# Kernel optimization log

Hardware: AMD Instinct MI355X
Metric: run time of the kernel (lower is better)

The kernel has to match this reference:

```python
import jax, jax.numpy as jnp
import numpy as np

B, T, C = 4, 2048, 1024
N_HEAD = 16
HEAD = C // N_HEAD

def setup_inputs() -> dict:
    key = jax.random.key(0)
    k1, k2, k3 = jax.random.split(key, 3)
    x = jax.random.normal(k1, (B, T, C), dtype=jnp.float32)
    w_attn = jax.random.normal(k2, (C, 3 * C), dtype=jnp.float32) * (1.0 / np.sqrt(C))
    w_proj = jax.random.normal(k3, (C, C), dtype=jnp.float32) * (1.0 / np.sqrt(C))
    return {"x": x, "w_attn": w_attn, "w_proj": w_proj}

def reference(x, w_attn, w_proj):
    b, t, c = x.shape
    qkv = x @ w_attn  # [B,T,3C]
    q, k, v = jnp.split(qkv, 3, axis=-1)
    # [B,T,C] -> [B,H,T,D]
    def heads(z):
        return z.reshape(b, t, N_HEAD, HEAD).transpose(0, 2, 1, 3)
    q, k, v = heads(q), heads(k), heads(v)
    scale = 1.0 / np.sqrt(HEAD)
    att = jnp.einsum('bhqd,bhkd->bhqk', q, k) * scale  # [B,H,T,T]
    causal = jnp.tril(jnp.ones((t, t), dtype=bool))
    att = jnp.where(causal[None, None], att, -jnp.inf)
    att = jax.nn.softmax(att, axis=-1)
    y = jnp.einsum('bhqk,bhkd->bhqd', att, v)  # [B,H,T,D]
    y = y.transpose(0, 2, 1, 3).reshape(b, t, c)
    return y @ w_proj
```

## Files before the change

### kernel.cpp

```cpp
#include <hip/hip_runtime.h>
#include <hip/hip_bf16.h>


typedef __attribute__((ext_vector_type(8))) short bf16x8;
typedef __attribute__((ext_vector_type(4))) float f32x4;
typedef __attribute__((ext_vector_type(16))) float f32x16;

#define T_DIM 2048
#define NHEAD 16
#define HDIM  64

__device__ __forceinline__ unsigned short f2bf(float f) {
    union { float f; unsigned int u; } v; v.f = f;
    unsigned int r = v.u + 0x7fffu + ((v.u >> 16) & 1u);
    return (unsigned short)(r >> 16);
}

__device__ __forceinline__ unsigned cvtpk_bf16(float lo, float hi) {
    unsigned r;
    asm("v_cvt_pk_bf16_f32 %0, %1, %2" : "=v"(r) : "v"(lo), "v"(hi));
    return r;
}
__device__ __forceinline__ void pl32swap(unsigned &x, unsigned &y) {
    asm("v_permlane32_swap_b32 %0, %1" : "+v"(x), "+v"(y));
}
__device__ __forceinline__ bf16x8 mk8(unsigned w0, unsigned w1, unsigned w2, unsigned w3) {
    union { unsigned u[4]; bf16x8 v; } p;
    p.u[0] = w0; p.u[1] = w1; p.u[2] = w2; p.u[3] = w3;
    return p.v;
}

__device__ __forceinline__ void gload_lds16(const void* g, void* l) {
    __builtin_amdgcn_global_load_lds(
        (const __attribute__((address_space(1))) void*)g,
        (__attribute__((address_space(3))) void*)l,
        16, 0, 0);
}

__global__ void cvt_bf16_k(const float* __restrict__ src, unsigned short* __restrict__ dst, int n) {
    int i = (blockIdx.x * blockDim.x + threadIdx.x) * 4;
    if (i < n) {
        float4 v = *(const float4*)(src + i);
        ushort4 o; o.x = f2bf(v.x); o.y = f2bf(v.y); o.z = f2bf(v.z); o.w = f2bf(v.w);
        *(ushort4*)(dst + i) = o;
    }
}

__global__ void transpose_wb_k(const float* __restrict__ src, unsigned short* __restrict__ dst,
                               int R, int Cc) {
    __shared__ float tile[32][33];
    int c0 = blockIdx.x * 32, r0 = blockIdx.y * 32;
    int tx = threadIdx.x & 31, ty = threadIdx.x >> 5;
    #pragma unroll
    for (int i = 0; i < 32; i += 8)
        tile[ty + i][tx] = src[(size_t)(r0 + ty + i) * Cc + c0 + tx];
    __syncthreads();
    #pragma unroll
    for (int i = 0; i < 32; i += 8)
        dst[(size_t)(c0 + ty + i) * R + r0 + tx] = f2bf(tile[tx][ty + i]);
}

template<int EPI>
__global__ __launch_bounds__(512, 2) void gemm_bt_k(
    const unsigned short* __restrict__ A, const unsigned short* __restrict__ Bt,
    void* __restrict__ out0, void* __restrict__ out1, void* __restrict__ out2,
    int M, int N, int K)
{
    extern __shared__ __align__(16) unsigned short smem[];
    unsigned short* sA = smem;
    unsigned short* sB = smem + 49152;

    const int tid = threadIdx.x, lane = tid & 63, wave = tid >> 6;
    const int wm = wave >> 1, wn = wave & 1;
    const int lrow = lane & 15, hi = lane >> 4;

    const int nwg = gridDim.x * gridDim.y;
    const int lin = blockIdx.y * gridDim.x + blockIdx.x;
    const int lin2 = (lin & 7) * (nwg >> 3) + (lin >> 3);
    const int bxg = lin2 % gridDim.x, byg = lin2 / gridDim.x;
    const int row0 = byg * 256, col0 = bxg * 128;

    const int arow = tid >> 3;
    const int gk = ((tid & 7) ^ (arow & 7)) * 8;
    const unsigned short* gA0 = A + (size_t)(row0 + arow) * K + gk;
    const unsigned short* gA1 = A + (size_t)(row0 + arow + 64) * K + gk;
    const unsigned short* gA2 = A + (size_t)(row0 + arow + 128) * K + gk;
    const unsigned short* gA3 = A + (size_t)(row0 + arow + 192) * K + gk;
    const unsigned short* gB0 = Bt + (size_t)(col0 + arow) * K + gk;
    const unsigned short* gB1 = Bt + (size_t)(col0 + arow + 64) * K + gk;

    const int NT = K >> 6;

#define STAGE(ts, sl) { const size_t ko_ = (size_t)(ts) * 64; \
        unsigned short* dA_ = sA + (sl) * 16384; \
        unsigned short* dB_ = sB + (sl) * 8192; \
        gload_lds16(gA0 + ko_, dA_ + tid * 8); \
        gload_lds16(gA1 + ko_, dA_ + (tid + 512) * 8); \
        gload_lds16(gA2 + ko_, dA_ + (tid + 1024) * 8); \
        gload_lds16(gA3 + ko_, dA_ + (tid + 1536) * 8); \
        gload_lds16(gB0 + ko_, dB_ + tid * 8); \
        gload_lds16(gB1 + ko_, dB_ + (tid + 512) * 8); }

    f32x4 acc[4][4] = {};

    STAGE(0, 0);
    STAGE(1, 1);
    asm volatile("s_waitcnt vmcnt(6)" ::: "memory");
    __builtin_amdgcn_s_barrier();
    __builtin_amdgcn_sched_barrier(0);

    int slot = 0;
    for (int t = 0; t < NT; ++t) {
        if (t + 2 < NT) {
            const int s2 = (slot + 2 >= 3) ? slot - 1 : slot + 2;
            STAGE(t + 2, s2);
        }
        const unsigned short* As = sA + slot * 16384;
        const unsigned short* Bs = sB + slot * 8192;
        bf16x8 af[2][4], bf_[2][4];
        #pragma unroll
        for (int ks = 0; ks < 2; ++ks) {
            const int kc = (ks * 4 + hi) ^ (lrow & 7);
            #pragma unroll
            for (int mi = 0; mi < 4; ++mi)
                af[ks][mi] = *(const bf16x8*)&As[((wm * 64 + mi * 16 + lrow) * 8 + kc) * 8];
            #pragma unroll
            for (int ni = 0; ni < 4; ++ni)
                bf_[ks][ni] = *(const bf16x8*)&Bs[((wn * 64 + ni * 16 + lrow) * 8 + kc) * 8];
        }
        __builtin_amdgcn_s_setprio(1);
        #pragma unroll
        for (int ks = 0; ks < 2; ++ks)
            #pragma unroll
            for (int mi = 0; mi < 4; ++mi)
                #pragma unroll
                for (int ni = 0; ni < 4; ++ni)
                    acc[mi][ni] = __builtin_amdgcn_mfma_f32_16x16x32_bf16(af[ks][mi], bf_[ks][ni], acc[mi][ni], 0, 0, 0);
        __builtin_amdgcn_s_setprio(0);
        if (t + 2 < NT) { asm volatile("s_waitcnt vmcnt(6)" ::: "memory"); }
        else           { asm volatile("s_waitcnt vmcnt(0)" ::: "memory"); }
        __builtin_amdgcn_s_barrier();
        __builtin_amdgcn_sched_barrier(0);
        slot = (slot + 1 >= 3) ? 0 : slot + 1;
    }
#undef STAGE

    if (EPI == 1) {
        #pragma unroll
        for (int mi = 0; mi < 4; ++mi)
            #pragma unroll
            for (int ni = 0; ni < 4; ++ni) {
                int gm0 = row0 + wm * 64 + mi * 16 + hi * 4;
                int gn  = col0 + wn * 64 + ni * 16 + lrow;
                #pragma unroll
                for (int r = 0; r < 4; ++r)
                    ((float*)out0)[(size_t)(gm0 + r) * N + gn] = acc[mi][ni][r];
            }
    } else if (col0 < 1024) {
        const int bb = row0 >> 11;
        #pragma unroll
        for (int mi = 0; mi < 4; ++mi)
            #pragma unroll
            for (int ni = 0; ni < 4; ++ni) {
                int gm0 = row0 + wm * 64 + mi * 16 + hi * 4;
                int gn  = col0 + wn * 64 + ni * 16 + lrow;
                int h = (gn >> 6) & 15, d = gn & 63;
                #pragma unroll
                for (int r = 0; r < 4; ++r) {
                    int t = (gm0 + r) & 2047;
                    ((unsigned short*)out0)[((size_t)(bb * NHEAD + h) * T_DIM + t) * HDIM + d] =
                        f2bf(acc[mi][ni][r] * 0.18033688011112042f);
                }
            }
    } else {
        const bool isK = (col0 < 2048);
        unsigned short* st = smem;
        __syncthreads();
        #pragma unroll
        for (int mi = 0; mi < 4; ++mi) {
            #pragma unroll
            for (int ni = 0; ni < 4; ++ni) {
                const int gnl = wn * 64 + ni * 16 + lrow;
                const int hl = gnl >> 6, d = gnl & 63;
                #pragma unroll
                for (int r = 0; r < 4; ++r) {
                    const int tl = wm * 64 + mi * 16 + hi * 4 + r;
                    int idx;
                    if (isK) idx = (hl * 4 + (tl >> 6)) * 4096 + ((d >> 3) * 64 + (tl & 63)) * 8 + (d & 7);
                    else     idx = (hl * 4 + (tl >> 6)) * 4096 + (((tl >> 3) & 7) * 64 + d) * 8 + (tl & 7);
                    st[idx] = f2bf(acc[mi][ni][r]);
                }
            }
        }
        __syncthreads();
        unsigned short* outb = (unsigned short*)(isK ? out1 : out2);
        const int bb = row0 >> 11;
        const int h0 = (col0 & 1023) >> 6;
        const int tc0 = (row0 & 2047) >> 6;
        #pragma unroll
        for (int seg = 0; seg < 8; ++seg) {
            const int hl = seg >> 2, tc = seg & 3;
            const size_t gbase = ((size_t)(bb * NHEAD + h0 + hl) * 32 + tc0 + tc) * 4096;
            *(uint4*)(outb + gbase + tid * 8) = *(const uint4*)(st + seg * 4096 + tid * 8);
        }
    }
}

__global__ __launch_bounds__(512) void attn_k(
    const unsigned short* __restrict__ qb, const unsigned short* __restrict__ kcm,
    const unsigned short* __restrict__ vcm, unsigned short* __restrict__ yb)
{
    __shared__ __align__(16) unsigned short Ks[2][4096];
    __shared__ __align__(16) unsigned short Vs[2][4096];

    const int tid = threadIdx.x, lane = tid & 63, wave = tid >> 6;
    const int bh = blockIdx.y;
    const int q32 = lane & 31, hi32 = lane >> 5;
    const unsigned short* Kg = kcm + (size_t)bh * 32 * 4096;
    const unsigned short* Vg = vcm + (size_t)bh * 32 * 4096;

    #pragma unroll
    for (int pass = 0; pass < 2; ++pass) {
        const int bxx = (pass == 0) ? (int)blockIdx.x : (7 - (int)blockIdx.x);
        const int ntiles = 4 * bxx + 4;
        const int q0w = bxx * 256 + wave * 32;
        const int qg = q0w + q32;

        const unsigned short* qrow = qb + ((size_t)bh * T_DIM + q0w + q32) * HDIM;
        bf16x8 qf[4];
        #pragma unroll
        for (int kc = 0; kc < 4; ++kc)
            qf[kc] = *(const bf16x8*)(qrow + kc * 16 + hi32 * 8);

        f32x16 o0 = {}, o1 = {};
        float lsum = 0.f;

        gload_lds16(Kg + tid * 8, &Ks[0][tid * 8]);
        gload_lds16(Vg + tid * 8, &Vs[0][tid * 8]);
        __syncthreads();

        int cur = 0;
        for (int jt = 0; jt < ntiles; ++jt) {
            if (jt + 1 < ntiles) {
                gload_lds16(Kg + (size_t)(jt + 1) * 4096 + tid * 8, &Ks[cur ^ 1][tid * 8]);
                gload_lds16(Vg + (size_t)(jt + 1) * 4096 + tid * 8, &Vs[cur ^ 1][tid * 8]);
            }
            if (jt * 64 <= q0w + 31) {
                f32x16 s0 = {}, s1 = {};
                #pragma unroll
                for (int kc = 0; kc < 4; ++kc) {
                    bf16x8 a0 = *(const bf16x8*)&Ks[cur][((kc * 2 + hi32) * 64 + q32) * 8];
                    bf16x8 a1 = *(const bf16x8*)&Ks[cur][((kc * 2 + hi32) * 64 + 32 + q32) * 8];
                    s0 = __builtin_amdgcn_mfma_f32_32x32x16_bf16(a0, qf[kc], s0, 0, 0, 0);
                    s1 = __builtin_amdgcn_mfma_f32_32x32x16_bf16(a1, qf[kc], s1, 0, 0, 0);
                }
                if (jt * 64 + 63 > q0w) {
                    #pragma unroll
                    for (int r = 0; r < 16; ++r) {
                        int kv0 = jt * 64 + (r & 3) + 8 * (r >> 2) + 4 * hi32;
                        if (kv0 > qg)      s0[r] = -1e30f;
                        if (kv0 + 32 > qg) s1[r] = -1e30f;
                    }
                }
                bf16x8 pa[4];
                #pragma unroll
                for (int blk = 0; blk < 2; ++blk) {
                    float p_[16]; unsigned w_[8];
                    #pragma unroll
                    for (int i = 0; i < 16; ++i) {
                        float sv = blk ? s1[i] : s0[i];
                        p_[i] = __builtin_amdgcn_exp2f(sv - 16.0f);
                        lsum += p_[i];
                    }
                    #pragma unroll
                    for (int i = 0; i < 8; ++i) w_[i] = cvtpk_bf16(p_[2 * i], p_[2 * i + 1]);
                    pl32swap(w_[0], w_[2]); pl32swap(w_[1], w_[3]);
                    pl32swap(w_[4], w_[6]); pl32swap(w_[5], w_[7]);
                    pa[blk * 2]     = mk8(w_[0], w_[1], w_[2], w_[3]);
                    pa[blk * 2 + 1] = mk8(w_[4], w_[5], w_[6], w_[7]);
                }
                #pragma unroll
                for (int kvc = 0; kvc < 4; ++kvc) {
                    bf16x8 b0 = *(const bf16x8*)&Vs[cur][((kvc * 2 + hi32) * 64 + q32) * 8];
                    bf16x8 b1 = *(const bf16x8*)&Vs[cur][((kvc * 2 + hi32) * 64 + 32 + q32) * 8];
                    o0 = __builtin_amdgcn_mfma_f32_32x32x16_bf16(pa[kvc], b0, o0, 0, 0, 0);
                    o1 = __builtin_amdgcn_mfma_f32_32x32x16_bf16(pa[kvc], b1, o1, 0, 0, 0);
                }
            }
            __syncthreads();
            cur ^= 1;
        }

        {
            unsigned la = __float_as_uint(lsum), lb = __float_as_uint(lsum);
            pl32swap(la, lb);
            lsum = __uint_as_float(la) + __uint_as_float(lb);
        }
        const int bb2 = bh >> 4, h = bh & 15;
        #pragma unroll
        for (int r = 0; r < 16; ++r) {
            const int cr = (r & 3) + 8 * (r >> 2) + 4 * hi32;
            float inv = 1.0f / __shfl(lsum, cr);
            int t = q0w + cr;
            size_t off = ((size_t)(bb2 * T_DIM + t)) * 1024 + h * HDIM + q32;
            yb[off]      = f2bf(o0[r] * inv);
            yb[off + 32] = f2bf(o1[r] * inv);
        }
    }
}

extern "C" void kernel_launch(void* const* d_in, const int* in_sizes, int n_in,
                              void* d_out, int out_size, void* d_ws, size_t ws_size,
                              hipStream_t stream) {
    const float* x      = (const float*)d_in[0];
    const float* w_attn = (const float*)d_in[1];
    const float* w_proj = (const float*)d_in[2];
    float* out = (float*)d_out;

    unsigned short* xb  = (unsigned short*)d_ws;
    unsigned short* wat = xb  + (size_t)8192 * 1024;
    unsigned short* wpt = wat + (size_t)3072 * 1024;
    unsigned short* qb  = wpt + (size_t)1024 * 1024;
    unsigned short* kcm = qb  + (size_t)64 * 2048 * 64;
    unsigned short* vcm = kcm + (size_t)64 * 2048 * 64;
    unsigned short* yb  = vcm + (size_t)64 * 2048 * 64;

    (void)hipFuncSetAttribute((const void*)gemm_bt_k<0>,
                              hipFuncAttributeMaxDynamicSharedMemorySize, 147456);
    (void)hipFuncSetAttribute((const void*)gemm_bt_k<1>,
                              hipFuncAttributeMaxDynamicSharedMemorySize, 147456);

    cvt_bf16_k<<<8192, 256, 0, stream>>>(x, xb, 8192 * 1024);
    transpose_wb_k<<<dim3(96, 32), 256, 0, stream>>>(w_attn, wat, 1024, 3072);
    transpose_wb_k<<<dim3(32, 32), 256, 0, stream>>>(w_proj, wpt, 1024, 1024);

    gemm_bt_k<0><<<dim3(24, 32), 512, 147456, stream>>>(xb, wat, qb, kcm, vcm, 8192, 3072, 1024);
    attn_k<<<dim3(4, 64), 512, 0, stream>>>(qb, kcm, vcm, yb);
    gemm_bt_k<1><<<dim3(8, 32), 512, 147456, stream>>>(yb, wpt, out, nullptr, nullptr, 8192, 1024, 1024);
}
```

Before: 168.9 us.

## Split GEMM K-step into two half-phases interleaving LDS reads, global prefetch and MFMA

```diff
diff --git a/kernel.cpp b/kernel.cpp
--- a/kernel.cpp
+++ b/kernel.cpp
@@ -91,51 +91,74 @@
 
     const int NT = K >> 6;
 
-#define STAGE(ts, sl) { const size_t ko_ = (size_t)(ts) * 64; \
+#define STAGE_P0(ts, sl) { const size_t ko_ = (size_t)(ts) * 64; \
+        unsigned short* dA_ = sA + (sl) * 16384; \
+        gload_lds16(gA0 + ko_, dA_ + tid * 8); \
+        gload_lds16(gA1 + ko_, dA_ + (tid + 512) * 8); \
+        gload_lds16(gA2 + ko_, dA_ + (tid + 1024) * 8); }
+#define STAGE_P1(ts, sl) { const size_t ko_ = (size_t)(ts) * 64; \
         unsigned short* dA_ = sA + (sl) * 16384; \
         unsigned short* dB_ = sB + (sl) * 8192; \
-        gload_lds16(gA0 + ko_, dA_ + tid * 8); \
-        gload_lds16(gA1 + ko_, dA_ + (tid + 512) * 8); \
-        gload_lds16(gA2 + ko_, dA_ + (tid + 1024) * 8); \
         gload_lds16(gA3 + ko_, dA_ + (tid + 1536) * 8); \
         gload_lds16(gB0 + ko_, dB_ + tid * 8); \
         gload_lds16(gB1 + ko_, dB_ + (tid + 512) * 8); }
 
     f32x4 acc[4][4] = {};
 
-    STAGE(0, 0);
-    STAGE(1, 1);
+    STAGE_P0(0, 0); STAGE_P1(0, 0);
+    STAGE_P0(1, 1); STAGE_P1(1, 1);
     asm volatile("s_waitcnt vmcnt(6)" ::: "memory");
     __builtin_amdgcn_s_barrier();
     __builtin_amdgcn_sched_barrier(0);
 
     int slot = 0;
     for (int t = 0; t < NT; ++t) {
-        if (t + 2 < NT) {
-            const int s2 = (slot + 2 >= 3) ? slot - 1 : slot + 2;
-            STAGE(t + 2, s2);
-        }
+        const int s2 = (slot + 2 >= 3) ? slot - 1 : slot + 2;
         const unsigned short* As = sA + slot * 16384;
         const unsigned short* Bs = sB + slot * 8192;
-        bf16x8 af[2][4], bf_[2][4];
-        #pragma unroll
-        for (int ks = 0; ks < 2; ++ks) {
-            const int kc = (ks * 4 + hi) ^ (lrow & 7);
+        bf16x8 af[4], bf_[4];
+
+        {
+            const int kc = hi ^ (lrow & 7);
             #pragma unroll
             for (int mi = 0; mi < 4; ++mi)
-                af[ks][mi] = *(const bf16x8*)&As[((wm * 64 + mi * 16 + lrow) * 8 + kc) * 8];
+                af[mi] = *(const bf16x8*)&As[((wm * 64 + mi * 16 + lrow) * 8 + kc) * 8];
             #pragma unroll
             for (int ni = 0; ni < 4; ++ni)
-                bf_[ks][ni] = *(const bf16x8*)&Bs[((wn * 64 + ni * 16 + lrow) * 8 + kc) * 8];
-        }
+                bf_[ni] = *(const bf16x8*)&Bs[((wn * 64 + ni * 16 + lrow) * 8 + kc) * 8];
+        }
+        if (t + 2 < NT) STAGE_P0(t + 2, s2);
+        __builtin_amdgcn_s_barrier();
+        asm volatile("s_waitcnt lgkmcnt(0)" ::: "memory");
+        __builtin_amdgcn_sched_barrier(0);
         __builtin_amdgcn_s_setprio(1);
         #pragma unroll
-        for (int ks = 0; ks < 2; ++ks)
+        for (int mi = 0; mi < 4; ++mi)
+            #pragma unroll
+            for (int ni = 0; ni < 4; ++ni)
+                acc[mi][ni] = __builtin_amdgcn_mfma_f32_16x16x32_bf16(af[mi], bf_[ni], acc[mi][ni], 0, 0, 0);
+        __builtin_amdgcn_s_setprio(0);
+        __builtin_amdgcn_s_barrier();
+
+        {
+            const int kc = (4 + hi) ^ (lrow & 7);
             #pragma unroll
             for (int mi = 0; mi < 4; ++mi)
-                #pragma unroll
-                for (int ni = 0; ni < 4; ++ni)
-                    acc[mi][ni] = __builtin_amdgcn_mfma_f32_16x16x32_bf16(af[ks][mi], bf_[ks][ni], acc[mi][ni], 0, 0, 0);
+                af[mi] = *(const bf16x8*)&As[((wm * 64 + mi * 16 + lrow) * 8 + kc) * 8];
+            #pragma unroll
+            for (int ni = 0; ni < 4; ++ni)
+                bf_[ni] = *(const bf16x8*)&Bs[((wn * 64 + ni * 16 + lrow) * 8 + kc) * 8];
+        }
+        if (t + 2 < NT) STAGE_P1(t + 2, s2);
+        __builtin_amdgcn_s_barrier();
+        asm volatile("s_waitcnt lgkmcnt(0)" ::: "memory");
+        __builtin_amdgcn_sched_barrier(0);
+        __builtin_amdgcn_s_setprio(1);
+        #pragma unroll
+        for (int mi = 0; mi < 4; ++mi)
+            #pragma unroll
+            for (int ni = 0; ni < 4; ++ni)
+                acc[mi][ni] = __builtin_amdgcn_mfma_f32_16x16x32_bf16(af[mi], bf_[ni], acc[mi][ni], 0, 0, 0);
         __builtin_amdgcn_s_setprio(0);
         if (t + 2 < NT) { asm volatile("s_waitcnt vmcnt(6)" ::: "memory"); }
         else           { asm volatile("s_waitcnt vmcnt(0)" ::: "memory"); }
@@ -143,7 +166,8 @@
         __builtin_amdgcn_sched_barrier(0);
         slot = (slot + 1 >= 3) ? 0 : slot + 1;
     }
-#undef STAGE
+#undef STAGE_P0
+#undef STAGE_P1
 
     if (EPI == 1) {
         #pragma unroll
```

Result: no change. 167.5 us (-0.8%).

## Shrink GEMM tiles to 128x128 with 256 threads and drop triple-buffered pipeline

Applied to the files above, without the earlier changes.

```diff
diff --git a/kernel.cpp b/kernel.cpp
--- a/kernel.cpp
+++ b/kernel.cpp
@@ -61,14 +61,14 @@
 }
 
 template<int EPI>
-__global__ __launch_bounds__(512, 2) void gemm_bt_k(
+__global__ __launch_bounds__(256) void gemm_bt_k(
     const unsigned short* __restrict__ A, const unsigned short* __restrict__ Bt,
     void* __restrict__ out0, void* __restrict__ out1, void* __restrict__ out2,
     int M, int N, int K)
 {
-    extern __shared__ __align__(16) unsigned short smem[];
+    __shared__ __align__(16) unsigned short smem[16384];
     unsigned short* sA = smem;
-    unsigned short* sB = smem + 49152;
+    unsigned short* sB = smem + 8192;
 
     const int tid = threadIdx.x, lane = tid & 63, wave = tid >> 6;
     const int wm = wave >> 1, wn = wave & 1;
@@ -78,55 +78,40 @@
     const int lin = blockIdx.y * gridDim.x + blockIdx.x;
     const int lin2 = (lin & 7) * (nwg >> 3) + (lin >> 3);
     const int bxg = lin2 % gridDim.x, byg = lin2 / gridDim.x;
-    const int row0 = byg * 256, col0 = bxg * 128;
+    const int row0 = byg * 128, col0 = bxg * 128;
 
     const int arow = tid >> 3;
     const int gk = ((tid & 7) ^ (arow & 7)) * 8;
-    const unsigned short* gA0 = A + (size_t)(row0 + arow) * K + gk;
-    const unsigned short* gA1 = A + (size_t)(row0 + arow + 64) * K + gk;
-    const unsigned short* gA2 = A + (size_t)(row0 + arow + 128) * K + gk;
-    const unsigned short* gA3 = A + (size_t)(row0 + arow + 192) * K + gk;
-    const unsigned short* gB0 = Bt + (size_t)(col0 + arow) * K + gk;
-    const unsigned short* gB1 = Bt + (size_t)(col0 + arow + 64) * K + gk;
+    const unsigned short* gA = A  + (size_t)(row0 + arow) * K + gk;
+    const unsigned short* gB = Bt + (size_t)(col0 + arow) * K + gk;
 
     const int NT = K >> 6;
 
-#define STAGE(ts, sl) { const size_t ko_ = (size_t)(ts) * 64; \
-        unsigned short* dA_ = sA + (sl) * 16384; \
-        unsigned short* dB_ = sB + (sl) * 8192; \
-        gload_lds16(gA0 + ko_, dA_ + tid * 8); \
-        gload_lds16(gA1 + ko_, dA_ + (tid + 512) * 8); \
-        gload_lds16(gA2 + ko_, dA_ + (tid + 1024) * 8); \
-        gload_lds16(gA3 + ko_, dA_ + (tid + 1536) * 8); \
-        gload_lds16(gB0 + ko_, dB_ + tid * 8); \
-        gload_lds16(gB1 + ko_, dB_ + (tid + 512) * 8); }
+#define STAGE(t) { const size_t ko_ = (size_t)(t) * 64; \
+        gload_lds16(gA + ko_,                   sA + tid * 8); \
+        gload_lds16(gA + (size_t)32 * K + ko_,  sA + (tid + 256) * 8); \
+        gload_lds16(gA + (size_t)64 * K + ko_,  sA + (tid + 512) * 8); \
+        gload_lds16(gA + (size_t)96 * K + ko_,  sA + (tid + 768) * 8); \
+        gload_lds16(gB + ko_,                   sB + tid * 8); \
+        gload_lds16(gB + (size_t)32 * K + ko_,  sB + (tid + 256) * 8); \
+        gload_lds16(gB + (size_t)64 * K + ko_,  sB + (tid + 512) * 8); \
+        gload_lds16(gB + (size_t)96 * K + ko_,  sB + (tid + 768) * 8); }
 
     f32x4 acc[4][4] = {};
 
-    STAGE(0, 0);
-    STAGE(1, 1);
-    asm volatile("s_waitcnt vmcnt(6)" ::: "memory");
-    __builtin_amdgcn_s_barrier();
-    __builtin_amdgcn_sched_barrier(0);
-
-    int slot = 0;
     for (int t = 0; t < NT; ++t) {
-        if (t + 2 < NT) {
-            const int s2 = (slot + 2 >= 3) ? slot - 1 : slot + 2;
-            STAGE(t + 2, s2);
-        }
-        const unsigned short* As = sA + slot * 16384;
-        const unsigned short* Bs = sB + slot * 8192;
+        STAGE(t);
+        __syncthreads();
         bf16x8 af[2][4], bf_[2][4];
         #pragma unroll
         for (int ks = 0; ks < 2; ++ks) {
             const int kc = (ks * 4 + hi) ^ (lrow & 7);
             #pragma unroll
             for (int mi = 0; mi < 4; ++mi)
-                af[ks][mi] = *(const bf16x8*)&As[((wm * 64 + mi * 16 + lrow) * 8 + kc) * 8];
+                af[ks][mi] = *(const bf16x8*)&sA[((wm * 64 + mi * 16 + lrow) * 8 + kc) * 8];
             #pragma unroll
             for (int ni = 0; ni < 4; ++ni)
-                bf_[ks][ni] = *(const bf16x8*)&Bs[((wn * 64 + ni * 16 + lrow) * 8 + kc) * 8];
+                bf_[ks][ni] = *(const bf16x8*)&sB[((wn * 64 + ni * 16 + lrow) * 8 + kc) * 8];
         }
         __builtin_amdgcn_s_setprio(1);
         #pragma unroll
@@ -137,11 +122,7 @@
                 for (int ni = 0; ni < 4; ++ni)
                     acc[mi][ni] = __builtin_amdgcn_mfma_f32_16x16x32_bf16(af[ks][mi], bf_[ks][ni], acc[mi][ni], 0, 0, 0);
         __builtin_amdgcn_s_setprio(0);
-        if (t + 2 < NT) { asm volatile("s_waitcnt vmcnt(6)" ::: "memory"); }
-        else           { asm volatile("s_waitcnt vmcnt(0)" ::: "memory"); }
-        __builtin_amdgcn_s_barrier();
-        __builtin_amdgcn_sched_barrier(0);
-        slot = (slot + 1 >= 3) ? 0 : slot + 1;
+        __syncthreads();
     }
 #undef STAGE
 
@@ -174,7 +155,6 @@
             }
     } else {
         const bool isK = (col0 < 2048);
-        unsigned short* st = smem;
         __syncthreads();
         #pragma unroll
         for (int mi = 0; mi < 4; ++mi) {
@@ -186,22 +166,23 @@
                 for (int r = 0; r < 4; ++r) {
                     const int tl = wm * 64 + mi * 16 + hi * 4 + r;
                     int idx;
-                    if (isK) idx = (hl * 4 + (tl >> 6)) * 4096 + ((d >> 3) * 64 + (tl & 63)) * 8 + (d & 7);
-                    else     idx = (hl * 4 + (tl >> 6)) * 4096 + (((tl >> 3) & 7) * 64 + d) * 8 + (tl & 7);
-                    st[idx] = f2bf(acc[mi][ni][r]);
+                    if (isK) idx = (hl * 2 + (tl >> 6)) * 4096 + ((d >> 3) * 64 + (tl & 63)) * 8 + (d & 7);
+                    else     idx = (hl * 2 + (tl >> 6)) * 4096 + (((tl >> 3) & 7) * 64 + d) * 8 + (tl & 7);
+                    smem[idx] = f2bf(acc[mi][ni][r]);
                 }
             }
         }
         __syncthreads();
         unsigned short* outb = (unsigned short*)(isK ? out1 : out2);
         const int bb = row0 >> 11;
-        const int h0 = (col0 & 1023) >> 6;
+        const int h0 = ((col0 - (isK ? 1024 : 2048)) >> 6);
         const int tc0 = (row0 & 2047) >> 6;
         #pragma unroll
-        for (int seg = 0; seg < 8; ++seg) {
-            const int hl = seg >> 2, tc = seg & 3;
+        for (int seg = 0; seg < 4; ++seg) {
+            const int hl = seg >> 1, tc = seg & 1;
             const size_t gbase = ((size_t)(bb * NHEAD + h0 + hl) * 32 + tc0 + tc) * 4096;
-            *(uint4*)(outb + gbase + tid * 8) = *(const uint4*)(st + seg * 4096 + tid * 8);
+            *(uint4*)(outb + gbase + tid * 8)         = *(const uint4*)(smem + seg * 4096 + tid * 8);
+            *(uint4*)(outb + gbase + (tid + 256) * 8) = *(const uint4*)(smem + seg * 4096 + (tid + 256) * 8);
         }
     }
 }
@@ -325,16 +306,11 @@
     unsigned short* vcm = kcm + (size_t)64 * 2048 * 64;
     unsigned short* yb  = vcm + (size_t)64 * 2048 * 64;
 
-    (void)hipFuncSetAttribute((const void*)gemm_bt_k<0>,
-                              hipFuncAttributeMaxDynamicSharedMemorySize, 147456);
-    (void)hipFuncSetAttribute((const void*)gemm_bt_k<1>,
-                              hipFuncAttributeMaxDynamicSharedMemorySize, 147456);
-
     cvt_bf16_k<<<8192, 256, 0, stream>>>(x, xb, 8192 * 1024);
     transpose_wb_k<<<dim3(96, 32), 256, 0, stream>>>(w_attn, wat, 1024, 3072);
     transpose_wb_k<<<dim3(32, 32), 256, 0, stream>>>(w_proj, wpt, 1024, 1024);
 
-    gemm_bt_k<0><<<dim3(24, 32), 512, 147456, stream>>>(xb, wat, qb, kcm, vcm, 8192, 3072, 1024);
+    gemm_bt_k<0><<<dim3(24, 64), 256, 0, stream>>>(xb, wat, qb, kcm, vcm, 8192, 3072, 1024);
     attn_k<<<dim3(4, 64), 512, 0, stream>>>(qb, kcm, vcm, yb);
-    gemm_bt_k<1><<<dim3(8, 32), 512, 147456, stream>>>(yb, wpt, out, nullptr, nullptr, 8192, 1024, 1024);
-}
+    gemm_bt_k<1><<<dim3(8, 64), 256, 0, stream>>>(yb, wpt, out, nullptr, nullptr, 8192, 1024, 1024);
+}
```

Result: no change. 166.5 us (-1.4%).
